# Kernel optimization log

Measured on AMD Instinct MI355X. Metric: run time of the kernel, lower is better.

## Reference

```python
import jax, jax.numpy as jnp
import numpy as np

B = 2          # batch size (fixed constant; torch code derives it from coords[:,0].max()+1)
C = 64         # NUM_BEV_FEATURES
NX = NY = 480  # grid_size, nz == 1
NXC = NYC = 960  # hardcoded 'cen' grid


def _make_coords(key, P, b, ny, nx):
    kb, ky, kx = jax.random.split(key, 3)
    bi = jax.random.randint(kb, (P,), 0, b, dtype=jnp.int32)
    z = jnp.zeros((P,), jnp.int32)
    y = jax.random.randint(ky, (P,), 0, ny, dtype=jnp.int32)
    x = jax.random.randint(kx, (P,), 0, nx, dtype=jnp.int32)
    return jnp.stack([bi, z, y, x], axis=1)


def setup_inputs() -> dict:
    key = jax.random.key(0)
    ks = jax.random.split(key, 8)
    return {
        "radar_cen_pillar_features": jax.random.normal(ks[0], (8000, C), jnp.float32),
        "radar_cen_coords": _make_coords(ks[1], 8000, B, NYC, NXC),
        "lidar_cen_pillar_features": jax.random.normal(ks[2], (30000, C), jnp.float32),
        "lidar_cen_coords": _make_coords(ks[3], 30000, B, NYC, NXC),
        "lidar_pillar_features": jax.random.normal(ks[4], (30000, C), jnp.float32),
        "lidar_coords": _make_coords(ks[5], 30000, B, NY, NX),
        "radar_pillar_features": jax.random.normal(ks[6], (8000, C), jnp.float32),
        "radar_coords": _make_coords(ks[7], 8000, B, NY, NX),
    }


def _scatter_bev(feat, coords, ny, nx):
    # feat [P, C], coords [P, 4] = (b, z, y, x); flat index = z + y*nx + x (nz==1 so z==0)
    idx = coords[:, 1] + coords[:, 2] * nx + coords[:, 3]
    grid = jnp.zeros((B, ny * nx, feat.shape[1]), feat.dtype)
    grid = grid.at[coords[:, 0], idx].set(feat)
    # -> [B, C, ny, nx]
    return grid.transpose(0, 2, 1).reshape(B, feat.shape[1], ny, nx)


def _maxpool2(x):
    # AdaptiveMaxPool2d(480) on 960x960 == 2x2 max pool
    b, c, h, w = x.shape
    return x.reshape(b, c, h // 2, 2, w // 2, 2).max(axis=(3, 5))


def reference(radar_cen_pillar_features, radar_cen_coords,
              lidar_cen_pillar_features, lidar_cen_coords,
              lidar_pillar_features, lidar_coords,
              radar_pillar_features, radar_coords):
    radar_cen = _maxpool2(_scatter_bev(radar_cen_pillar_features, radar_cen_coords, NYC, NXC))
    lidar_cen = _maxpool2(_scatter_bev(lidar_cen_pillar_features, lidar_cen_coords, NYC, NXC))
    lidar = _scatter_bev(lidar_pillar_features, lidar_coords, NY, NX)
    radar = _scatter_bev(radar_pillar_features, radar_coords, NY, NX)
    cat = jnp.concatenate(
        [jnp.concatenate([lidar, lidar_cen], axis=1),
         jnp.concatenate([radar, radar_cen], axis=1)], axis=1)
    return lidar, radar, cat
```

## Files before the change

### kernel.cpp

```cpp
#include <hip/hip_runtime.h>

#define NX   480
#define NXC  960
#define NS   (480*480)
#define NSC  (960*960)
#define CC   64
#define BB   2

typedef float f4v __attribute__((ext_vector_type(4)));

__device__ __forceinline__ void nt_store4(float* p, float a, float b, float c, float d) {
    f4v v = {a, b, c, d};
    __builtin_nontemporal_store(v, (f4v*)p);
}

__device__ __forceinline__ f4v ld4(int w, const float* __restrict__ f, int c) {
    f4v z = {0.0f, 0.0f, 0.0f, 0.0f};
    if (w < 0) return z;
    return *(const f4v*)(f + (size_t)w * CC + c);
}

__device__ __forceinline__ f4v max4(f4v a, f4v b) {
    f4v r;
    r.x = fmaxf(a.x, b.x); r.y = fmaxf(a.y, b.y);
    r.z = fmaxf(a.z, b.z); r.w = fmaxf(a.w, b.w);
    return r;
}

struct SrcDesc { const int* coords; int* winner; int P; int nx; int ns; };

__global__ void __launch_bounds__(256)
scatter_winner4(SrcDesc s0, SrcDesc s1, SrcDesc s2, SrcDesc s3) {
    SrcDesc d = (blockIdx.y == 0) ? s0 : (blockIdx.y == 1) ? s1
              : (blockIdx.y == 2) ? s2 : s3;
    int p = blockIdx.x * 256 + threadIdx.x;
    if (p >= d.P) return;
    int b = d.coords[4*p + 0];
    int y = d.coords[4*p + 2];
    int x = d.coords[4*p + 3];
    atomicMax(&d.winner[b*d.ns + y*d.nx + x], p);
}

__global__ void __launch_bounds__(256)
dense_direct(const float* __restrict__ lf, const float* __restrict__ rf,
             const int* __restrict__ wl, const int* __restrict__ wr,
             float* __restrict__ out_l, float* __restrict__ out_r,
             float* __restrict__ out_cat)
{
    int s = (blockIdx.x * 256 + threadIdx.x) * 4;
    int b = blockIdx.y;
    int z = blockIdx.z;

    const float* f = z ? rf : lf;
    const int*   w = z ? wr : wl;

    int4 v = *(const int4*)(w + (size_t)b*NS + s);
    int wa[4] = {v.x, v.y, v.z, v.w};

    float* o1 = (z ? out_r : out_l) + (size_t)b*CC*NS + s;
    float* o2 = out_cat + (size_t)b*256*NS + (size_t)(z ? 128 : 0)*NS + s;

    #pragma unroll 2
    for (int g = 0; g < 16; ++g) {
        int c = g * 4;
        f4v x0 = ld4(wa[0], f, c);
        f4v x1 = ld4(wa[1], f, c);
        f4v x2 = ld4(wa[2], f, c);
        f4v x3 = ld4(wa[3], f, c);
        #pragma unroll
        for (int k = 0; k < 4; ++k) {
            size_t cs = (size_t)(c + k) * NS;
            nt_store4(o1 + cs, x0[k], x1[k], x2[k], x3[k]);
            nt_store4(o2 + cs, x0[k], x1[k], x2[k], x3[k]);
        }
    }
}

__global__ void __launch_bounds__(256)
dense_cen(const float* __restrict__ lcf, const float* __restrict__ rcf,
          const int* __restrict__ wlc, const int* __restrict__ wrc,
          float* __restrict__ out_cat)
{
    int s = (blockIdx.x * 256 + threadIdx.x) * 4;
    int b = blockIdx.y;
    int z = blockIdx.z;

    const float* f = z ? rcf : lcf;
    const int*   w = z ? wrc : wlc;

    int py = s / NX, px = s - py * NX;
    int y0 = py * 2, x0 = px * 2;
    const int* wb = w + (size_t)b * NSC;
    int4 t0 = *(const int4*)(wb + (size_t)y0*NXC + x0);
    int4 t1 = *(const int4*)(wb + (size_t)y0*NXC + x0 + 4);
    int4 b0 = *(const int4*)(wb + (size_t)(y0+1)*NXC + x0);
    int4 b1 = *(const int4*)(wb + (size_t)(y0+1)*NXC + x0 + 4);
    int wt[8] = {t0.x, t0.y, t0.z, t0.w, t1.x, t1.y, t1.z, t1.w};
    int wbm[8] = {b0.x, b0.y, b0.z, b0.w, b1.x, b1.y, b1.z, b1.w};

    float* o2 = out_cat + (size_t)b*256*NS + (size_t)(z ? 192 : 64)*NS + s;

    #pragma unroll 1
    for (int g = 0; g < 16; ++g) {
        int c = g * 4;
        f4v a[4];
        #pragma unroll
        for (int j = 0; j < 4; ++j) {
            f4v m = ld4(wt[2*j], f, c);
            m = max4(m, ld4(wt[2*j+1],  f, c));
            m = max4(m, ld4(wbm[2*j],   f, c));
            m = max4(m, ld4(wbm[2*j+1], f, c));
            a[j] = m;
        }
        #pragma unroll
        for (int k = 0; k < 4; ++k) {
            size_t cs = (size_t)(c + k) * NS;
            nt_store4(o2 + cs, a[0][k], a[1][k], a[2][k], a[3][k]);
        }
    }
}

extern "C" void kernel_launch(void* const* d_in, const int* in_sizes, int n_in,
                              void* d_out, int out_size, void* d_ws, size_t ws_size,
                              hipStream_t stream) {
    const float* rc_feat   = (const float*)d_in[0];
    const int*   rc_coords = (const int*)  d_in[1];
    const float* lc_feat   = (const float*)d_in[2];
    const int*   lc_coords = (const int*)  d_in[3];
    const float* l_feat    = (const float*)d_in[4];
    const int*   l_coords  = (const int*)  d_in[5];
    const float* r_feat    = (const float*)d_in[6];
    const int*   r_coords  = (const int*)  d_in[7];

    int P_rc = in_sizes[0] / CC;
    int P_lc = in_sizes[2] / CC;
    int P_l  = in_sizes[4] / CC;
    int P_r  = in_sizes[6] / CC;

    float* out_lidar = (float*)d_out;
    float* out_radar = out_lidar + (size_t)BB*CC*NS;
    float* out_cat   = out_radar + (size_t)BB*CC*NS;

    int* w_l  = (int*)d_ws;
    int* w_r  = w_l  + BB*NS;
    int* w_lc = w_r  + BB*NS;
    int* w_rc = w_lc + BB*NSC;
    size_t ws_bytes = (size_t)(2*BB*NS + 2*BB*NSC) * sizeof(int);

    hipMemsetAsync(d_ws, 0xFF, ws_bytes, stream);

    SrcDesc s_l  = { l_coords,  w_l,  P_l,  NX,  NS  };
    SrcDesc s_r  = { r_coords,  w_r,  P_r,  NX,  NS  };
    SrcDesc s_lc = { lc_coords, w_lc, P_lc, NXC, NSC };
    SrcDesc s_rc = { rc_coords, w_rc, P_rc, NXC, NSC };
    int maxP = max(max(P_l, P_r), max(P_lc, P_rc));
    dim3 wgrid((maxP + 255) / 256, 4);
    scatter_winner4<<<wgrid, 256, 0, stream>>>(s_l, s_r, s_lc, s_rc);

    dim3 grid(NS / (256 * 4), BB, 2);
    dense_direct<<<grid, 256, 0, stream>>>(l_feat, r_feat, w_l, w_r,
                                           out_lidar, out_radar, out_cat);
    dense_cen<<<grid, 256, 0, stream>>>(lc_feat, rc_feat, w_lc, w_rc, out_cat);
}
```

Before: 741.9 us.

## Fuse dense kernels into one channel-group sweep kernel with persistent spatial loops

Replaces the two dense expansion kernels with one kernel whose grid is (job, channel group, spatial segment). Each block handles four channels across a long strided range of pixels, looping 25 times and prefetching the next winner indices. The aim is to cut launch overhead and make each block's stores land in a few contiguous channel planes. The cost is that winner indices are now re-read once per channel group, 16 times in total. The grid is also small (1152 blocks), which may limit memory-level parallelism.

```diff
diff --git a/kernel.cpp b/kernel.cpp
--- a/kernel.cpp
+++ b/kernel.cpp
@@ -42,80 +42,70 @@
 }
 
 __global__ void __launch_bounds__(256)
-dense_direct(const float* __restrict__ lf, const float* __restrict__ rf,
-             const int* __restrict__ wl, const int* __restrict__ wr,
-             float* __restrict__ out_l, float* __restrict__ out_r,
-             float* __restrict__ out_cat)
+dense_sweep(const float* __restrict__ lf,  const float* __restrict__ rf,
+            const float* __restrict__ lcf, const float* __restrict__ rcf,
+            const int* __restrict__ wl,  const int* __restrict__ wr,
+            const int* __restrict__ wlc, const int* __restrict__ wrc,
+            float* __restrict__ out_l, float* __restrict__ out_r,
+            float* __restrict__ out_cat)
 {
-    int s = (blockIdx.x * 256 + threadIdx.x) * 4;
-    int b = blockIdx.y;
-    int z = blockIdx.z;
+    int job = blockIdx.x;
+    int c   = blockIdx.y * 4;
+    int seg = blockIdx.z;
+    int t   = threadIdx.x;
 
-    const float* f = z ? rf : lf;
-    const int*   w = z ? wr : wl;
+    if (job < 4) {
+        int b = job >> 1, z = job & 1;
+        const float* f = z ? rf : lf;
+        const int*   w = (z ? wr : wl) + (size_t)b * NS;
+        float* o1 = (z ? out_r : out_l) + (size_t)b*CC*NS  + (size_t)c*NS;
+        float* o2 = out_cat + (size_t)b*256*NS + (size_t)((z ? 128 : 0) + c)*NS;
 
-    int4 v = *(const int4*)(w + (size_t)b*NS + s);
-    int wa[4] = {v.x, v.y, v.z, v.w};
+        int s0 = seg * 25600 + t * 4;
+        int4 wv = *(const int4*)(w + s0);
+        for (int st = 0; st < 25; ++st) {
+            int s = s0 + st * 1024;
+            int4 wc = wv;
+            if (st + 1 < 25) wv = *(const int4*)(w + s + 1024);
+            f4v x0 = ld4(wc.x, f, c);
+            f4v x1 = ld4(wc.y, f, c);
+            f4v x2 = ld4(wc.z, f, c);
+            f4v x3 = ld4(wc.w, f, c);
+            #pragma unroll
+            for (int k = 0; k < 4; ++k) {
+                size_t cs = (size_t)k * NS + s;
+                nt_store4(o1 + cs, x0[k], x1[k], x2[k], x3[k]);
+                nt_store4(o2 + cs, x0[k], x1[k], x2[k], x3[k]);
+            }
+        }
+    } else {
+        int b = (job - 4) >> 1, z = (job - 4) & 1;
+        const float* f = z ? rcf : lcf;
+        const int*   w = (z ? wrc : wlc) + (size_t)b * NSC;
+        float* o2 = out_cat + (size_t)b*256*NS + (size_t)((z ? 192 : 64) + c)*NS;
 
-    float* o1 = (z ? out_r : out_l) + (size_t)b*CC*NS + s;
-    float* o2 = out_cat + (size_t)b*256*NS + (size_t)(z ? 128 : 0)*NS + s;
-
-    #pragma unroll 2
-    for (int g = 0; g < 16; ++g) {
-        int c = g * 4;
-        f4v x0 = ld4(wa[0], f, c);
-        f4v x1 = ld4(wa[1], f, c);
-        f4v x2 = ld4(wa[2], f, c);
-        f4v x3 = ld4(wa[3], f, c);
-        #pragma unroll
-        for (int k = 0; k < 4; ++k) {
-            size_t cs = (size_t)(c + k) * NS;
-            nt_store4(o1 + cs, x0[k], x1[k], x2[k], x3[k]);
-            nt_store4(o2 + cs, x0[k], x1[k], x2[k], x3[k]);
-        }
-    }
-}
-
-__global__ void __launch_bounds__(256)
-dense_cen(const float* __restrict__ lcf, const float* __restrict__ rcf,
-          const int* __restrict__ wlc, const int* __restrict__ wrc,
-          float* __restrict__ out_cat)
-{
-    int s = (blockIdx.x * 256 + threadIdx.x) * 4;
-    int b = blockIdx.y;
-    int z = blockIdx.z;
-
-    const float* f = z ? rcf : lcf;
-    const int*   w = z ? wrc : wlc;
-
-    int py = s / NX, px = s - py * NX;
-    int y0 = py * 2, x0 = px * 2;
-    const int* wb = w + (size_t)b * NSC;
-    int4 t0 = *(const int4*)(wb + (size_t)y0*NXC + x0);
-    int4 t1 = *(const int4*)(wb + (size_t)y0*NXC + x0 + 4);
-    int4 b0 = *(const int4*)(wb + (size_t)(y0+1)*NXC + x0);
-    int4 b1 = *(const int4*)(wb + (size_t)(y0+1)*NXC + x0 + 4);
-    int wt[8] = {t0.x, t0.y, t0.z, t0.w, t1.x, t1.y, t1.z, t1.w};
-    int wbm[8] = {b0.x, b0.y, b0.z, b0.w, b1.x, b1.y, b1.z, b1.w};
-
-    float* o2 = out_cat + (size_t)b*256*NS + (size_t)(z ? 192 : 64)*NS + s;
-
-    #pragma unroll 1
-    for (int g = 0; g < 16; ++g) {
-        int c = g * 4;
-        f4v a[4];
-        #pragma unroll
-        for (int j = 0; j < 4; ++j) {
-            f4v m = ld4(wt[2*j], f, c);
-            m = max4(m, ld4(wt[2*j+1],  f, c));
-            m = max4(m, ld4(wbm[2*j],   f, c));
-            m = max4(m, ld4(wbm[2*j+1], f, c));
-            a[j] = m;
-        }
-        #pragma unroll
-        for (int k = 0; k < 4; ++k) {
-            size_t cs = (size_t)(c + k) * NS;
-            nt_store4(o2 + cs, a[0][k], a[1][k], a[2][k], a[3][k]);
+        for (int st = 0; st < 25; ++st) {
+            int s = seg * 25600 + st * 1024 + t * 4;
+            int py = s / NX, px = s - py * NX;
+            const int* wr0 = w + (size_t)(py*2) * NXC + px*2;
+            int4 t0 = *(const int4*)(wr0);
+            int4 t1 = *(const int4*)(wr0 + 4);
+            int4 b0 = *(const int4*)(wr0 + NXC);
+            int4 b1 = *(const int4*)(wr0 + NXC + 4);
+            int wt[8]  = {t0.x, t0.y, t0.z, t0.w, t1.x, t1.y, t1.z, t1.w};
+            int wb2[8] = {b0.x, b0.y, b0.z, b0.w, b1.x, b1.y, b1.z, b1.w};
+            f4v a[4];
+            #pragma unroll
+            for (int j = 0; j < 4; ++j) {
+                f4v m = ld4(wt[2*j], f, c);
+                m = max4(m, ld4(wt[2*j+1],  f, c));
+                m = max4(m, ld4(wb2[2*j],   f, c));
+                m = max4(m, ld4(wb2[2*j+1], f, c));
+                a[j] = m;
+            }
+            #pragma unroll
+            for (int k = 0; k < 4; ++k)
+                nt_store4(o2 + (size_t)k * NS + s, a[0][k], a[1][k], a[2][k], a[3][k]);
         }
     }
 }
@@ -157,8 +147,8 @@
     dim3 wgrid((maxP + 255) / 256, 4);
     scatter_winner4<<<wgrid, 256, 0, stream>>>(s_l, s_r, s_lc, s_rc);
 
-    dim3 grid(NS / (256 * 4), BB, 2);
-    dense_direct<<<grid, 256, 0, stream>>>(l_feat, r_feat, w_l, w_r,
-                                           out_lidar, out_radar, out_cat);
-    dense_cen<<<grid, 256, 0, stream>>>(lc_feat, rc_feat, w_lc, w_rc, out_cat);
+    dim3 grid(8, 16, 9);
+    dense_sweep<<<grid, 256, 0, stream>>>(l_feat, r_feat, lc_feat, rc_feat,
+                                          w_l, w_r, w_lc, w_rc,
+                                          out_lidar, out_radar, out_cat);
 }
```

Result: slower. 805.5 us (+8.6%).
